# Kernel tuning notes

Hardware: AMD Instinct MI355X
Metric: run time of the kernel (lower is better)

Reference implementation:

```python
import jax, jax.numpy as jnp
import numpy as np

NC = 80
REG_MAX = 16
STRIDES = (8.0, 16.0, 32.0)
MAX_DET = 300
IOU_THR = 0.7
CONF_THR = 0.001
NCAND = 1024        # top candidates kept before greedy NMS
MAX_WH = 7680.0     # per-class offset trick (ultralytics max_wh)


def _make_anchors(shapes, strides, offset=0.5):
    pts, strs = [], []
    for (h, w), s in zip(shapes, strides):
        sx = jnp.arange(w, dtype=jnp.float32) + offset
        sy = jnp.arange(h, dtype=jnp.float32) + offset
        gy, gx = jnp.meshgrid(sy, sx, indexing='ij')
        pts.append(jnp.stack((gx, gy), -1).reshape(-1, 2))   # (h*w, 2)
        strs.append(jnp.full((h * w, 1), s, jnp.float32))
    return jnp.concatenate(pts, 0), jnp.concatenate(strs, 0)


def _decode_raw(feats):
    """feats_to_raw_yolov8: DFL decode + anchor transform -> pixel cxcywh + sigmoid cls."""
    B = feats[0].shape[0]
    no = 4 * REG_MAX + NC
    merged = jnp.concatenate([f.reshape(B, no, -1) for f in feats], axis=2)  # (B,no,A)
    dist, cls = merged[:, :4 * REG_MAX], merged[:, 4 * REG_MAX:]
    pd = dist.transpose(0, 2, 1).reshape(B, -1, 4, REG_MAX)                  # (B,A,4,reg_max)
    proj = jnp.arange(REG_MAX, dtype=merged.dtype)
    ltrb = jnp.einsum('bafr,r->baf', jax.nn.softmax(pd, -1), proj)           # (B,A,4)
    anchors, strd = _make_anchors([f.shape[2:] for f in feats], STRIDES)     # (A,2),(A,1)
    lt, rb = ltrb[..., :2], ltrb[..., 2:]
    x1y1 = anchors[None] - lt
    x2y2 = anchors[None] + rb
    cxy = (x1y1 + x2y2) * 0.5
    wh = x2y2 - x1y1
    dbox = jnp.concatenate((cxy, wh), -1) * strd[None]                       # (B,A,4) pixel cxcywh
    return dbox, jax.nn.sigmoid(cls).transpose(0, 2, 1)                      # (B,A,nc)


def _iou_one_vs_many(box, boxes):
    lt = jnp.maximum(box[:2], boxes[:, :2])
    rb = jnp.minimum(box[2:], boxes[:, 2:])
    inter = jnp.prod(jnp.clip(rb - lt, 0.0), -1)
    a1 = jnp.prod(box[2:] - box[:2])
    a2 = jnp.prod(boxes[:, 2:] - boxes[:, :2], -1)
    return inter / (a1 + a2 - inter + 1e-7)


def _nms_image(boxes_cxcywh, scores_cls):
    """conf threshold + per-class greedy NMS + max_det truncation -> (max_det, 6)."""
    conf = scores_cls.max(-1)                                   # (A,)
    cls = jnp.argmax(scores_cls, -1).astype(jnp.float32)        # (A,)
    conf = jnp.where(conf > CONF_THR, conf, 0.0)
    top_conf, idx = jax.lax.top_k(conf, NCAND)                  # candidate pre-selection
    cb = boxes_cxcywh[idx]                                      # (NCAND,4) cxcywh
    ccls = cls[idx]
    xy1 = cb[:, :2] - cb[:, 2:] * 0.5
    xy2 = cb[:, :2] + cb[:, 2:] * 0.5
    bx = jnp.concatenate((xy1, xy2), -1) + (ccls * MAX_WH)[:, None]  # class-offset xyxy

    def step(sc, _):
        j = jnp.argmax(sc)
        s = sc[j]
        sup = _iou_one_vs_many(bx[j], bx) > IOU_THR  # self-IoU=1 kills j as well
        return jnp.where(sup, 0.0, sc), (j, s)

    _, (sel, ss) = jax.lax.scan(step, top_conf, None, length=MAX_DET)
    rows = jnp.concatenate((cb[sel], ss[:, None], ccls[sel][:, None]), -1)  # (max_det,6)
    return jnp.where((ss > CONF_THR)[:, None], rows, 0.0)


def setup_inputs() -> dict:
    key = jax.random.key(0)
    k0, k1, k2 = jax.random.split(key, 3)
    B, no = 32, 4 * REG_MAX + NC
    return {
        'feat0': jax.random.normal(k0, (B, no, 80, 80), jnp.float32),
        'feat1': jax.random.normal(k1, (B, no, 40, 40), jnp.float32),
        'feat2': jax.random.normal(k2, (B, no, 20, 20), jnp.float32),
    }


def reference(feat0, feat1, feat2):
    dbox, ps = _decode_raw([feat0, feat1, feat2])        # (B,A,4), (B,A,nc)
    return jax.vmap(_nms_image)(dbox, ps)                # (B, max_det, 6)
```

## Files before the change

kernel.cpp:

```cpp
#include <hip/hip_runtime.h>
#include <stdint.h>

#define NCLS    80
#define NA_TOT  8400
#define NBATCH  32
#define MAXDET  300
#define SSORT   2048
#define RANKCAP 1536
#define CONFTHR 0.001f
#define TILES_PER_IMG 132

__device__ __forceinline__ float xla_expf(float in) {
  const float exp_hi = 88.3762626647950f;
  const float exp_lo = -88.3762626647949f;
  const float LOG2EF = 1.44269504088896341f;
  const float C1 = 0.693359375f;
  const float C2 = -2.12194440e-4f;
  const float p0 = 1.9875691500E-4f, p1 = 1.3981999507E-3f, p2 = 8.3334519073E-3f;
  const float p3 = 4.1665795894E-2f, p4 = 1.6666665459E-1f, p5 = 5.0000001201E-1f;
  float x = fminf(fmaxf(in, exp_lo), exp_hi);
  float fx = floorf(__fadd_rn(__fmul_rn(x, LOG2EF), 0.5f));
  float tmp = __fmul_rn(C1, fx);
  float z   = __fmul_rn(C2, fx);
  x = __fsub_rn(x, tmp);
  x = __fsub_rn(x, z);
  float y = __fadd_rn(__fmul_rn(x, p0), p1);
  y = __fadd_rn(__fmul_rn(y, x), p2);
  y = __fadd_rn(__fmul_rn(y, x), p3);
  y = __fadd_rn(__fmul_rn(y, x), p4);
  y = __fadd_rn(__fmul_rn(y, x), p5);
  y = __fadd_rn(__fmul_rn(y, __fmul_rn(x, x)), x);
  y = __fadd_rn(1.0f, y);
  int m = (int)fx;
  float s = __uint_as_float((uint32_t)(m + 127) << 23);
  float r = __fmul_rn(y, s);
  return fmaxf(r, in);
}

__device__ __forceinline__ float xla_sigmoid(float v) {
  float e = xla_expf(-v);
  float den = __fadd_rn(1.0f, e);
  return 1.0f / den;
}

__device__ __forceinline__ void gload_lds16(const float* gp, float* lp) {
  __builtin_amdgcn_global_load_lds(
      (const __attribute__((address_space(1))) void*)gp,
      (__attribute__((address_space(3))) void*)lp, 16, 0, 0);
}

__global__ __launch_bounds__(256) void yolo_decode_kernel(
    const float* __restrict__ f0, const float* __restrict__ f1,
    const float* __restrict__ f2,
    float4* __restrict__ oboxes, float* __restrict__ oconf,
    float* __restrict__ oclsf) {
  __shared__ float sm[144 * 64];
  int bx  = blockIdx.x;
  int b   = bx / TILES_PER_IMG;
  int r   = bx - b * TILES_PER_IMG;
  int tid = threadIdx.x;
  int lane = tid & 63;
  int wv   = tid >> 6;

  const float* base; int Alvl, W, a0, lvlbase; float stridef;
  if (r < 100)      { base = f0 + (size_t)b * (144 * 6400); W = 80; Alvl = 6400;
                      a0 = r * 64; stridef = 8.0f; lvlbase = 0; }
  else if (r < 125) { base = f1 + (size_t)b * (144 * 1600); W = 40; Alvl = 1600;
                      a0 = (r - 100) * 64; stridef = 16.0f; lvlbase = 6400; }
  else              { base = f2 + (size_t)b * (144 * 400);  W = 20; Alvl = 400;
                      int aa = (r - 125) * 64; a0 = (aa + 64 <= 400) ? aa : 336;
                      stridef = 32.0f; lvlbase = 8000; }

  #pragma unroll
  for (int qq = 0; qq < 9; ++qq) {
    int chunk = wv * 9 + qq;
    int c     = chunk * 4 + (lane >> 4);
    int s     = (c >> 4) & 3;
    int idx4  = (lane & 15) ^ (s << 2);
    const float* gp = base + (size_t)c * Alvl + a0 + idx4 * 4;
    gload_lds16(gp, sm + chunk * 256);
  }
  asm volatile("s_waitcnt vmcnt(0)" ::: "memory");
  __builtin_amdgcn_s_barrier();

  const float* S = sm;
  int idx = tid >> 2;
  int w   = tid & 3;
  int ai  = a0 + idx;
  float ax = __fadd_rn((float)(ai % W), 0.5f);
  float ay = __fadd_rn((float)(ai / W), 0.5f);

  int sidx = idx ^ (w << 4);
  float d[16];
  float mx = -INFINITY;
  #pragma unroll
  for (int rr = 0; rr < 16; ++rr) {
    d[rr] = S[(w * 16 + rr) * 64 + sidx];
    mx = fmaxf(mx, d[rr]);
  }
  float e[16]; float ssum = 0.0f;
  #pragma unroll
  for (int rr = 0; rr < 16; ++rr) {
    e[rr] = xla_expf(__fsub_rn(d[rr], mx));
    ssum = __fadd_rn(ssum, e[rr]);
  }
  float acc = 0.0f;
  #pragma unroll
  for (int rr = 0; rr < 16; ++rr) {
    float p = e[rr] / ssum;
    acc = __fadd_rn(acc, __fmul_rn(p, (float)rr));
  }

  int l0 = lane & ~3;
  float lt0 = __shfl(acc, l0 + 0);
  float lt1 = __shfl(acc, l0 + 1);
  float lt2 = __shfl(acc, l0 + 2);
  float lt3 = __shfl(acc, l0 + 3);

  float best = -INFINITY, second = -INFINITY; int bi = 0;
  #pragma unroll 5
  for (int kk = 0; kk < 20; ++kk) {
    int c = 64 + w * 20 + kk;
    float v = S[c * 64 + (idx ^ (((c >> 4) & 3) << 4))];
    if (v > best)        { second = best; best = v; bi = w * 20 + kk; }
    else if (v > second) { second = v; }
  }
  float gb = __shfl(best, l0 + 0), gs = __shfl(second, l0 + 0);
  int   gi = __shfl(bi,   l0 + 0);
  #pragma unroll
  for (int qq = 1; qq < 4; ++qq) {
    float bq = __shfl(best, l0 + qq), sq = __shfl(second, l0 + qq);
    int   iq = __shfl(bi,   l0 + qq);
    if (bq > gb) { gs = fmaxf(gb, sq); gb = bq; gi = iq; }
    else         { gs = fmaxf(gs, bq); }
  }

  float conf = 0.0f; int cls = gi;
  if (__fsub_rn(gb, gs) < 1e-4f || gb > 5.0f) {
    if (w == 0) {
      float bs = -INFINITY; int bj = 0;
      for (int kk = 0; kk < NCLS; ++kk) {
        int c = 64 + kk;
        float v = S[c * 64 + (idx ^ (((c >> 4) & 3) << 4))];
        float s2 = xla_sigmoid(v);
        if (s2 > bs) { bs = s2; bj = kk; }
      }
      conf = bs; cls = bj;
    }
  } else {
    conf = xla_sigmoid(gb);
  }

  if (w == 0) {
    float x1 = __fsub_rn(ax, lt0);
    float y1 = __fsub_rn(ay, lt1);
    float x2 = __fadd_rn(ax, lt2);
    float y2 = __fadd_rn(ay, lt3);
    float cx = __fmul_rn(__fadd_rn(x1, x2), 0.5f);
    float cy = __fmul_rn(__fadd_rn(y1, y2), 0.5f);
    float ww = __fsub_rn(x2, x1);
    float hh = __fsub_rn(y2, y1);
    int t = b * NA_TOT + lvlbase + a0 + idx;
    oboxes[t] = make_float4(__fmul_rn(cx, stridef), __fmul_rn(cy, stridef),
                            __fmul_rn(ww, stridef), __fmul_rn(hh, stridef));
    conf = (conf > CONFTHR) ? conf : 0.0f;
    oconf[t] = conf;
    oclsf[t] = (float)cls;
  }
}

struct __align__(16) K2Lds {
  unsigned long long sortkeys[SSORT];
  unsigned confL[NA_TOT];
  unsigned hist[16][257];
  unsigned tot[257];
  unsigned Tarr[257];
};

__global__ __launch_bounds__(1024) void yolo_select_kernel(
    const float4* __restrict__ boxes, const float* __restrict__ conf,
    const float* __restrict__ clsf,
    float* __restrict__ g_rowd, unsigned long long* __restrict__ g_clsMask) {
  __shared__ K2Lds u;
  __shared__ unsigned s_need, s_prefix, s_found, s_B, s_scnt, s_cut, s_done;
  int b    = blockIdx.x;
  int tid  = threadIdx.x;
  int lane = tid & 63;
  int wv   = tid >> 6;
  const unsigned* confu = (const unsigned*)conf + (size_t)b * NA_TOT;
  float* rowd = g_rowd + (size_t)b * 1024 * 8;
  unsigned long long* cm = g_clsMask + (size_t)b * (NCLS * 16);

  for (int i = tid; i < NA_TOT; i += 1024) u.confL[i] = confu[i];
  {
    float4 z4 = make_float4(0.f, 0.f, 0.f, 0.f);
    float4* gr = (float4*)rowd;
    for (int k = tid; k < 2048; k += 1024) gr[k] = z4;
  }
  for (int i = tid; i < NCLS * 16; i += 1024) cm[i] = 0ull;
  if (tid == 0) { s_need = 1024; s_prefix = 0; s_cut = 0; s_done = 0; s_scnt = 0; }
  __syncthreads();

  for (int lv = 0; lv < 4; ++lv) {
    __syncthreads();
    if (s_done) break;
    for (int i = tid; i < 16 * 257; i += 1024) ((unsigned*)u.hist)[i] = 0;
    if (tid == 0) { s_found = 0; s_B = 0; }
    __syncthreads();
    unsigned pfx = s_prefix;
    for (int it = 0; it < 9; ++it) {
      int i = tid + it * 1024;
      unsigned c = (i < NA_TOT) ? u.confL[i] : 0u;
      bool in; unsigned bin;
      if (lv == 0)      { in = true;                bin = c >> 23; }
      else if (lv == 1) { in = ((c >> 23) == pfx);  bin = (c >> 15) & 0xFF; }
      else if (lv == 2) { in = ((c >> 15) == pfx);  bin = (c >> 7) & 0xFF; }
      else              { in = ((c >> 7)  == pfx);  bin = c & 0x7F; }
      bool act = (c != 0) && in;
      unsigned long long ab = __ballot(act);
      if (ab) {
        int fl = __ffsll(ab) - 1;
        unsigned fbin = __shfl(bin, fl);
        unsigned long long same = __ballot(act && (bin == fbin));
        if (same == ab) {
          if (lane == fl) atomicAdd(&u.hist[wv][fbin], (unsigned)__popcll(ab));
        } else if (act) {
          atomicAdd(&u.hist[wv][bin], 1u);
        }
      }
    }
    __syncthreads();
    if (tid < 256) {
      unsigned s = 0;
      #pragma unroll
      for (int q = 0; q < 16; ++q) s += u.hist[q][tid];
      u.tot[tid] = s;
    }
    __syncthreads();
    if (tid < 64) {
      unsigned carry = 0;
      if (tid == 0) u.Tarr[256] = 0;
      for (int ch = 3; ch >= 0; --ch) {
        int bb = ch * 64 + tid;
        unsigned v = u.tot[bb];
        #pragma unroll
        for (int off = 1; off < 64; off <<= 1) {
          unsigned t2 = __shfl_down(v, off);
          if (tid + off < 64) v += t2;
        }
        u.Tarr[bb] = v + carry;
        carry += __shfl(v, 0);
      }
    }
    __syncthreads();
    unsigned need = s_need;
    if (tid < 256) {
      unsigned h = u.tot[tid];
      if (h > 0 && u.Tarr[tid + 1] < need && u.Tarr[tid + 1] + h >= need) {
        s_B = (unsigned)tid; s_found = 1;
      }
    }
    __syncthreads();
    if (tid == 0) {
      if (!s_found) { s_cut = 1; s_done = 1; }
      else {
        unsigned B = s_B;
        unsigned selcnt = (1024u - need) + u.Tarr[B];
        if (selcnt <= (unsigned)RANKCAP || lv == 3) {
          s_done = 1;
          if (lv == 0)      s_cut = B << 23;
          else if (lv == 1) s_cut = (s_prefix << 23) | (B << 15);
          else if (lv == 2) s_cut = (s_prefix << 15) | (B << 7);
          else              s_cut = (s_prefix << 7)  | B;
        } else {
          s_need   = need - u.Tarr[B + 1];
          s_prefix = (s_prefix << 8) | B;
        }
      }
    }
  }
  __syncthreads();

  unsigned cut = s_cut;
  for (int it = 0; it < 9; ++it) {
    int i = tid + it * 1024;
    unsigned c = (i < NA_TOT) ? u.confL[i] : 0u;
    bool sel = (c != 0 && c >= cut);
    unsigned long long bal = __ballot(sel);
    unsigned base2 = 0;
    if (lane == 0 && bal) base2 = atomicAdd(&s_scnt, (unsigned)__popcll(bal));
    base2 = __shfl(base2, 0);
    if (sel) {
      unsigned p = base2 + (unsigned)__popcll(bal & ((1ull << lane) - 1ull));
      if (p < SSORT)
        u.sortkeys[p] = ((unsigned long long)c << 32) |
                        (unsigned long long)(0xFFFFFFFFu - (unsigned)i);
    }
  }
  __syncthreads();
  unsigned scnt = s_scnt; if (scnt > SSORT) scnt = SSORT;
  unsigned snp = (scnt + 1u) & ~1u;
  if (tid == 0 && (scnt & 1u)) u.sortkeys[scnt] = 0ull;
  __syncthreads();

  for (unsigned e = tid; e < scnt; e += 1024) {
    unsigned long long mykey = u.sortkeys[e];
    unsigned r = 0;
    #pragma unroll 4
    for (unsigned j = 0; j < snp; j += 2) {
      ulonglong2 kk = *reinterpret_cast<const ulonglong2*>(&u.sortkeys[j]);
      r += (kk.x > mykey) ? 1u : 0u;
      r += (kk.y > mykey) ? 1u : 0u;
    }
    if (r < 1024) {
      unsigned a = 0xFFFFFFFFu - (unsigned)(mykey & 0xFFFFFFFFull);
      float4 cb = boxes[(size_t)b * NA_TOT + a];
      float cls = clsf[(size_t)b * NA_TOT + a];
      float4* gr = (float4*)(rowd + (size_t)r * 8);
      gr[0] = cb;
      gr[1] = make_float4(__uint_as_float((unsigned)(mykey >> 32)), cls, 0.f, 0.f);
      atomicOr(&cm[(int)cls * 16 + (r >> 6)], 1ull << (r & 63));
    }
  }
}

struct K3Lds {
  unsigned long long rows[1024][16];
  float    rowdata[1024][6];
  unsigned long long am[16];
};

__global__ __launch_bounds__(1024) void yolo_nms_kernel(
    const float* __restrict__ g_rowd,
    const unsigned long long* __restrict__ g_clsMask,
    float* __restrict__ out) {
  __shared__ K3Lds u;
  __shared__ unsigned s_sticky, s_fill;
  int b    = blockIdx.x;
  int tid  = threadIdx.x;
  const unsigned long long* cm = g_clsMask + (size_t)b * (NCLS * 16);

  {
    const float4* gr = (const float4*)(g_rowd + ((size_t)b * 1024 + tid) * 8);
    float4 v0 = gr[0];
    float4 v1 = gr[1];
    u.rowdata[tid][0] = v0.x; u.rowdata[tid][1] = v0.y;
    u.rowdata[tid][2] = v0.z; u.rowdata[tid][3] = v0.w;
    u.rowdata[tid][4] = v1.x; u.rowdata[tid][5] = v1.y;
  }
  {
    unsigned long long* flat = &u.rows[0][0];
    for (int k = tid; k < 1024 * 16; k += 1024) flat[k] = 0ull;
  }
  if (tid < 16) u.am[tid] = 0ull;
  if (tid == 0) { s_sticky = 0xFFFFFFFFu; s_fill = 0; }
  __syncthreads();

  {
    float cls = u.rowdata[tid][5];
    int c = (int)cls;
    const unsigned long long* cmask = cm + c * 16;
    bool valid = (cmask[tid >> 6] >> (tid & 63)) & 1ull;
    if (valid) {
      float bx0 = u.rowdata[tid][0], by0 = u.rowdata[tid][1];
      float bw0 = u.rowdata[tid][2], bh0 = u.rowdata[tid][3];
      float off = __fmul_rn(cls, 7680.0f);
      float hw  = __fmul_rn(bw0, 0.5f), hh = __fmul_rn(bh0, 0.5f);
      float wx1 = __fadd_rn(__fsub_rn(bx0, hw), off);
      float wy1 = __fadd_rn(__fsub_rn(by0, hh), off);
      float wx2 = __fadd_rn(__fadd_rn(bx0, hw), off);
      float wy2 = __fadd_rn(__fadd_rn(by0, hh), off);
      float a1  = __fmul_rn(__fsub_rn(wx2, wx1), __fsub_rn(wy2, wy1));
      int sw = tid & 15;
      for (int q = 0; q < 16; ++q) {
        unsigned long long m = cmask[q];
        while (m) {
          int bit = __ffsll(m) - 1;
          m &= m - 1ull;
          int j = q * 64 + bit;
          float jx = u.rowdata[j][0], jy = u.rowdata[j][1];
          float jw = u.rowdata[j][2], jh = u.rowdata[j][3];
          float jhw = __fmul_rn(jw, 0.5f), jhh = __fmul_rn(jh, 0.5f);
          float jx1 = __fadd_rn(__fsub_rn(jx, jhw), off);
          float jy1 = __fadd_rn(__fsub_rn(jy, jhh), off);
          float jx2 = __fadd_rn(__fadd_rn(jx, jhw), off);
          float jy2 = __fadd_rn(__fadd_rn(jy, jhh), off);
          float ltx = fmaxf(wx1, jx1), lty = fmaxf(wy1, jy1);
          float rbx = fminf(wx2, jx2), rby = fminf(wy2, jy2);
          float iw = fmaxf(__fsub_rn(rbx, ltx), 0.0f);
          float ih = fmaxf(__fsub_rn(rby, lty), 0.0f);
          float inter = __fmul_rn(iw, ih);
          float a2 = __fmul_rn(__fsub_rn(jx2, jx1), __fsub_rn(jy2, jy1));
          float den = __fadd_rn(__fsub_rn(__fadd_rn(a1, a2), inter), 1e-7f);
          float iou = inter / den;
          if (iou > 0.7f)
            u.rows[tid][(j >> 6) ^ sw] |= (1ull << (j & 63));
        }
      }
    }
  }
  __syncthreads();

  if (tid < NCLS) {
    const unsigned long long* cmask = cm + tid * 16;
    unsigned long long alive[16];
    bool any = false;
    #pragma unroll
    for (int q = 0; q < 16; ++q) { alive[q] = cmask[q]; any |= (alive[q] != 0ull); }
    while (any) {
      int r = -1;
      #pragma unroll
      for (int q = 0; q < 16; ++q)
        if (r < 0 && alive[q]) r = q * 64 + (__ffsll(alive[q]) - 1);
      atomicOr(&u.am[r >> 6], 1ull << (r & 63));
      int sw = r & 15;
      unsigned long long selfw = u.rows[r][(r >> 6) ^ sw];
      bool selfbit = (selfw >> (r & 63)) & 1ull;
      if (!selfbit) { atomicMin(&s_sticky, (unsigned)r); break; }
      any = false;
      #pragma unroll
      for (int q = 0; q < 16; ++q) {
        alive[q] &= ~u.rows[r][q ^ sw];
        any |= (alive[q] != 0ull);
      }
    }
  }
  __syncthreads();

  unsigned rs = s_sticky;
  {
    unsigned r = (unsigned)tid;
    bool surv = (u.am[r >> 6] >> (r & 63)) & 1ull;
    if (surv && r <= rs) {
      unsigned e2 = 0;
      int hi = (int)(r >> 6);
      #pragma unroll
      for (int q = 0; q < 16; ++q) {
        unsigned long long m = u.am[q];
        if (q < hi)       e2 += (unsigned)__popcll(m);
        else if (q == hi) e2 += (unsigned)__popcll(m & ((1ull << (r & 63)) - 1ull));
      }
      if (e2 < MAXDET) {
        float* orow = out + (size_t)b * (MAXDET * 6) + (size_t)e2 * 6;
        orow[0] = u.rowdata[r][0];
        orow[1] = u.rowdata[r][1];
        orow[2] = u.rowdata[r][2];
        orow[3] = u.rowdata[r][3];
        orow[4] = u.rowdata[r][4];
        orow[5] = u.rowdata[r][5];
      }
    }
  }
  if (tid == 0) {
    unsigned fill;
    if (rs != 0xFFFFFFFFu) {
      unsigned es = 0;
      int hi = (int)(rs >> 6);
      #pragma unroll
      for (int q = 0; q < 16; ++q) {
        unsigned long long m = u.am[q];
        if (q < hi)       es += (unsigned)__popcll(m);
        else if (q == hi) es += (unsigned)__popcll(m & ((1ull << (rs & 63)) - 1ull));
      }
      fill = es + 1;
    } else {
      unsigned S = 0;
      #pragma unroll
      for (int q = 0; q < 16; ++q) S += (unsigned)__popcll(u.am[q]);
      fill = S;
    }
    s_fill = (fill > (unsigned)MAXDET) ? (unsigned)MAXDET : fill;
  }
  __syncthreads();

  {
    unsigned fill = s_fill;
    bool st = (rs != 0xFFFFFFFFu);
    float* orow = out + (size_t)b * (MAXDET * 6);
    for (int i = (int)fill * 6 + tid; i < MAXDET * 6; i += 1024) {
      float v = 0.0f;
      if (st) v = u.rowdata[rs][i - (i / 6) * 6];
      orow[i] = v;
    }
  }
}

extern "C" void kernel_launch(void* const* d_in, const int* in_sizes, int n_in,
                              void* d_out, int out_size, void* d_ws, size_t ws_size,
                              hipStream_t stream) {
  const float* f0 = (const float*)d_in[0];
  const float* f1 = (const float*)d_in[1];
  const float* f2 = (const float*)d_in[2];
  float* out = (float*)d_out;

  char* ws = (char*)d_ws;
  float4* boxes = (float4*)ws;
  float*  conf  = (float*)(ws + (size_t)NBATCH * NA_TOT * 16);
  float*  clsf  = (float*)(ws + (size_t)NBATCH * NA_TOT * 20);
  float*  rowd  = (float*)(ws + (size_t)NBATCH * NA_TOT * 24);
  unsigned long long* clsm =
      (unsigned long long*)(ws + (size_t)NBATCH * NA_TOT * 24 + 1048576);

  yolo_decode_kernel<<<NBATCH * TILES_PER_IMG, 256, 0, stream>>>(
      f0, f1, f2, boxes, conf, clsf);
  yolo_select_kernel<<<NBATCH, 1024, 0, stream>>>(boxes, conf, clsf, rowd, clsm);
  yolo_nms_kernel<<<NBATCH, 1024, 0, stream>>>(rowd, clsm, out);
}
```

Baseline: 136.8 us.

## Split rank-sort of candidates into separate kernel across 8 blocks per image

The O(n^2) rank counting of selected candidate keys moves out of the single-block-per-image select kernel into a new kernel that launches 8 blocks of 256 threads per image. Keys pass through a global workspace buffer instead of LDS. This spreads the quadratic ranking over many more CUs than the original 32 blocks could use. The cost is an extra kernel launch and key comparisons read from global memory or cache instead of LDS.

```diff
diff --git a/kernel.cpp b/kernel.cpp
--- a/kernel.cpp
+++ b/kernel.cpp
@@ -9,6 +9,7 @@
 #define RANKCAP 1536
 #define CONFTHR 0.001f
 #define TILES_PER_IMG 132
+#define GKCAP   2056
 
 __device__ __forceinline__ float xla_expf(float in) {
   const float exp_hi = 88.3762626647950f;
@@ -170,7 +171,6 @@
 }
 
 struct __align__(16) K2Lds {
-  unsigned long long sortkeys[SSORT];
   unsigned confL[NA_TOT];
   unsigned hist[16][257];
   unsigned tot[257];
@@ -178,8 +178,8 @@
 };
 
 __global__ __launch_bounds__(1024) void yolo_select_kernel(
-    const float4* __restrict__ boxes, const float* __restrict__ conf,
-    const float* __restrict__ clsf,
+    const float* __restrict__ conf,
+    unsigned long long* __restrict__ g_keys, unsigned* __restrict__ g_scnt,
     float* __restrict__ g_rowd, unsigned long long* __restrict__ g_clsMask) {
   __shared__ K2Lds u;
   __shared__ unsigned s_need, s_prefix, s_found, s_B, s_scnt, s_cut, s_done;
@@ -188,16 +188,16 @@
   int lane = tid & 63;
   int wv   = tid >> 6;
   const unsigned* confu = (const unsigned*)conf + (size_t)b * NA_TOT;
-  float* rowd = g_rowd + (size_t)b * 1024 * 8;
-  unsigned long long* cm = g_clsMask + (size_t)b * (NCLS * 16);
+  unsigned long long* gk = g_keys + (size_t)b * GKCAP;
 
   for (int i = tid; i < NA_TOT; i += 1024) u.confL[i] = confu[i];
   {
     float4 z4 = make_float4(0.f, 0.f, 0.f, 0.f);
-    float4* gr = (float4*)rowd;
+    float4* gr = (float4*)(g_rowd + (size_t)b * 1024 * 8);
     for (int k = tid; k < 2048; k += 1024) gr[k] = z4;
   }
-  for (int i = tid; i < NCLS * 16; i += 1024) cm[i] = 0ull;
+  for (int i = tid; i < NCLS * 16; i += 1024)
+    g_clsMask[(size_t)b * (NCLS * 16) + i] = 0ull;
   if (tid == 0) { s_need = 1024; s_prefix = 0; s_cut = 0; s_done = 0; s_scnt = 0; }
   __syncthreads();
 
@@ -293,34 +293,51 @@
     if (sel) {
       unsigned p = base2 + (unsigned)__popcll(bal & ((1ull << lane) - 1ull));
       if (p < SSORT)
-        u.sortkeys[p] = ((unsigned long long)c << 32) |
-                        (unsigned long long)(0xFFFFFFFFu - (unsigned)i);
-    }
-  }
-  __syncthreads();
-  unsigned scnt = s_scnt; if (scnt > SSORT) scnt = SSORT;
-  unsigned snp = (scnt + 1u) & ~1u;
-  if (tid == 0 && (scnt & 1u)) u.sortkeys[scnt] = 0ull;
-  __syncthreads();
-
-  for (unsigned e = tid; e < scnt; e += 1024) {
-    unsigned long long mykey = u.sortkeys[e];
-    unsigned r = 0;
-    #pragma unroll 4
-    for (unsigned j = 0; j < snp; j += 2) {
-      ulonglong2 kk = *reinterpret_cast<const ulonglong2*>(&u.sortkeys[j]);
-      r += (kk.x > mykey) ? 1u : 0u;
-      r += (kk.y > mykey) ? 1u : 0u;
-    }
-    if (r < 1024) {
-      unsigned a = 0xFFFFFFFFu - (unsigned)(mykey & 0xFFFFFFFFull);
-      float4 cb = boxes[(size_t)b * NA_TOT + a];
-      float cls = clsf[(size_t)b * NA_TOT + a];
-      float4* gr = (float4*)(rowd + (size_t)r * 8);
-      gr[0] = cb;
-      gr[1] = make_float4(__uint_as_float((unsigned)(mykey >> 32)), cls, 0.f, 0.f);
-      atomicOr(&cm[(int)cls * 16 + (r >> 6)], 1ull << (r & 63));
-    }
+        gk[p] = ((unsigned long long)c << 32) |
+                (unsigned long long)(0xFFFFFFFFu - (unsigned)i);
+    }
+  }
+  __syncthreads();
+  if (tid == 0) {
+    unsigned sc = s_scnt; if (sc > SSORT) sc = SSORT;
+    g_scnt[b] = sc;
+    if (sc & 1u) gk[sc] = 0ull;
+  }
+}
+
+__global__ __launch_bounds__(256) void yolo_rank_kernel(
+    const unsigned long long* __restrict__ g_keys,
+    const unsigned* __restrict__ g_scnt,
+    const float4* __restrict__ boxes, const float* __restrict__ clsf,
+    float* __restrict__ g_rowd, unsigned long long* __restrict__ g_clsMask) {
+  int bx   = blockIdx.x;
+  int b    = bx >> 3;
+  int part = bx & 7;
+  const unsigned long long* gk = g_keys + (size_t)b * GKCAP;
+  unsigned scnt = g_scnt[b];
+  unsigned snp  = (scnt + 1u) & ~1u;
+  unsigned e    = (unsigned)(part * 256 + threadIdx.x);
+  bool has = (e < scnt);
+  unsigned long long mykey = has ? gk[e] : 0ull;
+
+  unsigned r = 0;
+  #pragma unroll 4
+  for (unsigned j = 0; j < snp; j += 2) {
+    ulonglong2 kk = *reinterpret_cast<const ulonglong2*>(gk + j);
+    r += (kk.x > mykey) ? 1u : 0u;
+    r += (kk.y > mykey) ? 1u : 0u;
+  }
+
+  if (has && r < 1024) {
+    unsigned a = 0xFFFFFFFFu - (unsigned)(mykey & 0xFFFFFFFFull);
+    float4 cb = boxes[(size_t)b * NA_TOT + a];
+    float cls = clsf[(size_t)b * NA_TOT + a];
+    float* rowd = g_rowd + (size_t)b * 1024 * 8;
+    float4* gr = (float4*)(rowd + (size_t)r * 8);
+    gr[0] = cb;
+    gr[1] = make_float4(__uint_as_float((unsigned)(mykey >> 32)), cls, 0.f, 0.f);
+    atomicOr(&g_clsMask[(size_t)b * (NCLS * 16) + (int)cls * 16 + (r >> 6)],
+             1ull << (r & 63));
   }
 }
 
@@ -497,12 +514,17 @@
   float4* boxes = (float4*)ws;
   float*  conf  = (float*)(ws + (size_t)NBATCH * NA_TOT * 16);
   float*  clsf  = (float*)(ws + (size_t)NBATCH * NA_TOT * 20);
-  float*  rowd  = (float*)(ws + (size_t)NBATCH * NA_TOT * 24);
-  unsigned long long* clsm =
-      (unsigned long long*)(ws + (size_t)NBATCH * NA_TOT * 24 + 1048576);
+  size_t off = (size_t)NBATCH * NA_TOT * 24;
+  float*  rowd  = (float*)(ws + off);                 off += 1048576;
+  unsigned long long* clsm = (unsigned long long*)(ws + off); off += 327680;
+  unsigned long long* gkeys = (unsigned long long*)(ws + off); off += (size_t)NBATCH * GKCAP * 8;
+  unsigned* scnts = (unsigned*)(ws + off);
 
   yolo_decode_kernel<<<NBATCH * TILES_PER_IMG, 256, 0, stream>>>(
       f0, f1, f2, boxes, conf, clsf);
-  yolo_select_kernel<<<NBATCH, 1024, 0, stream>>>(boxes, conf, clsf, rowd, clsm);
+  yolo_select_kernel<<<NBATCH, 1024, 0, stream>>>(conf, gkeys, scnts,
+                                                  rowd, clsm);
+  yolo_rank_kernel<<<NBATCH * 8, 256, 0, stream>>>(gkeys, scnts, boxes, clsf,
+                                                   rowd, clsm);
   yolo_nms_kernel<<<NBATCH, 1024, 0, stream>>>(rowd, clsm, out);
 }
```

Result: slower. 152.0 us (+11.1%).

## Defer DFL box decode to only the top-1024 selected candidates

Applied to the files above, without the earlier changes.

The first kernel now reads only the 80 class channels and writes conf/class, skipping the 64 DFL distance channels for all 8400 anchors. A new kernel after selection runs the softmax-DFL decode only for the kept candidates, reading their 64 channels with strided gathers, and writes the box into the row buffer. The select kernel stores the anchor index in place of the box. This cuts decode-stage HBM traffic and exp work by roughly 44%, at the cost of an extra launch and uncoalesced per-candidate gathers.

```diff
diff --git a/kernel.cpp b/kernel.cpp
--- a/kernel.cpp
+++ b/kernel.cpp
@@ -49,12 +49,11 @@
       (__attribute__((address_space(3))) void*)lp, 16, 0, 0);
 }
 
-__global__ __launch_bounds__(256) void yolo_decode_kernel(
+__global__ __launch_bounds__(256) void yolo_confcls_kernel(
     const float* __restrict__ f0, const float* __restrict__ f1,
     const float* __restrict__ f2,
-    float4* __restrict__ oboxes, float* __restrict__ oconf,
-    float* __restrict__ oclsf) {
-  __shared__ float sm[144 * 64];
+    float* __restrict__ oconf, float* __restrict__ oclsf) {
+  __shared__ float sm[80 * 64];
   int bx  = blockIdx.x;
   int b   = bx / TILES_PER_IMG;
   int r   = bx - b * TILES_PER_IMG;
@@ -62,23 +61,22 @@
   int lane = tid & 63;
   int wv   = tid >> 6;
 
-  const float* base; int Alvl, W, a0, lvlbase; float stridef;
-  if (r < 100)      { base = f0 + (size_t)b * (144 * 6400); W = 80; Alvl = 6400;
-                      a0 = r * 64; stridef = 8.0f; lvlbase = 0; }
-  else if (r < 125) { base = f1 + (size_t)b * (144 * 1600); W = 40; Alvl = 1600;
-                      a0 = (r - 100) * 64; stridef = 16.0f; lvlbase = 6400; }
-  else              { base = f2 + (size_t)b * (144 * 400);  W = 20; Alvl = 400;
+  const float* base; int Alvl, a0, lvlbase;
+  if (r < 100)      { base = f0 + (size_t)b * (144 * 6400); Alvl = 6400;
+                      a0 = r * 64; lvlbase = 0; }
+  else if (r < 125) { base = f1 + (size_t)b * (144 * 1600); Alvl = 1600;
+                      a0 = (r - 100) * 64; lvlbase = 6400; }
+  else              { base = f2 + (size_t)b * (144 * 400);  Alvl = 400;
                       int aa = (r - 125) * 64; a0 = (aa + 64 <= 400) ? aa : 336;
-                      stridef = 32.0f; lvlbase = 8000; }
+                      lvlbase = 8000; }
 
   #pragma unroll
-  for (int qq = 0; qq < 9; ++qq) {
-    int chunk = wv * 9 + qq;
+  for (int qq = 0; qq < 5; ++qq) {
+    int chunk = wv * 5 + qq;
     int c     = chunk * 4 + (lane >> 4);
     int s     = (c >> 4) & 3;
     int idx4  = (lane & 15) ^ (s << 2);
-    const float* gp = base + (size_t)c * Alvl + a0 + idx4 * 4;
-    gload_lds16(gp, sm + chunk * 256);
+    gload_lds16(base + (size_t)(64 + c) * Alvl + a0 + idx4 * 4, sm + chunk * 256);
   }
   asm volatile("s_waitcnt vmcnt(0)" ::: "memory");
   __builtin_amdgcn_s_barrier();
@@ -86,45 +84,16 @@
   const float* S = sm;
   int idx = tid >> 2;
   int w   = tid & 3;
-  int ai  = a0 + idx;
-  float ax = __fadd_rn((float)(ai % W), 0.5f);
-  float ay = __fadd_rn((float)(ai / W), 0.5f);
-
-  int sidx = idx ^ (w << 4);
-  float d[16];
-  float mx = -INFINITY;
-  #pragma unroll
-  for (int rr = 0; rr < 16; ++rr) {
-    d[rr] = S[(w * 16 + rr) * 64 + sidx];
-    mx = fmaxf(mx, d[rr]);
-  }
-  float e[16]; float ssum = 0.0f;
-  #pragma unroll
-  for (int rr = 0; rr < 16; ++rr) {
-    e[rr] = xla_expf(__fsub_rn(d[rr], mx));
-    ssum = __fadd_rn(ssum, e[rr]);
-  }
-  float acc = 0.0f;
-  #pragma unroll
-  for (int rr = 0; rr < 16; ++rr) {
-    float p = e[rr] / ssum;
-    acc = __fadd_rn(acc, __fmul_rn(p, (float)rr));
-  }
-
-  int l0 = lane & ~3;
-  float lt0 = __shfl(acc, l0 + 0);
-  float lt1 = __shfl(acc, l0 + 1);
-  float lt2 = __shfl(acc, l0 + 2);
-  float lt3 = __shfl(acc, l0 + 3);
 
   float best = -INFINITY, second = -INFINITY; int bi = 0;
   #pragma unroll 5
   for (int kk = 0; kk < 20; ++kk) {
-    int c = 64 + w * 20 + kk;
+    int c = w * 20 + kk;
     float v = S[c * 64 + (idx ^ (((c >> 4) & 3) << 4))];
-    if (v > best)        { second = best; best = v; bi = w * 20 + kk; }
+    if (v > best)        { second = best; best = v; bi = c; }
     else if (v > second) { second = v; }
   }
+  int l0 = lane & ~3;
   float gb = __shfl(best, l0 + 0), gs = __shfl(second, l0 + 0);
   int   gi = __shfl(bi,   l0 + 0);
   #pragma unroll
@@ -140,8 +109,7 @@
     if (w == 0) {
       float bs = -INFINITY; int bj = 0;
       for (int kk = 0; kk < NCLS; ++kk) {
-        int c = 64 + kk;
-        float v = S[c * 64 + (idx ^ (((c >> 4) & 3) << 4))];
+        float v = S[kk * 64 + (idx ^ (((kk >> 4) & 3) << 4))];
         float s2 = xla_sigmoid(v);
         if (s2 > bs) { bs = s2; bj = kk; }
       }
@@ -152,17 +120,7 @@
   }
 
   if (w == 0) {
-    float x1 = __fsub_rn(ax, lt0);
-    float y1 = __fsub_rn(ay, lt1);
-    float x2 = __fadd_rn(ax, lt2);
-    float y2 = __fadd_rn(ay, lt3);
-    float cx = __fmul_rn(__fadd_rn(x1, x2), 0.5f);
-    float cy = __fmul_rn(__fadd_rn(y1, y2), 0.5f);
-    float ww = __fsub_rn(x2, x1);
-    float hh = __fsub_rn(y2, y1);
     int t = b * NA_TOT + lvlbase + a0 + idx;
-    oboxes[t] = make_float4(__fmul_rn(cx, stridef), __fmul_rn(cy, stridef),
-                            __fmul_rn(ww, stridef), __fmul_rn(hh, stridef));
     conf = (conf > CONFTHR) ? conf : 0.0f;
     oconf[t] = conf;
     oclsf[t] = (float)cls;
@@ -178,8 +136,7 @@
 };
 
 __global__ __launch_bounds__(1024) void yolo_select_kernel(
-    const float4* __restrict__ boxes, const float* __restrict__ conf,
-    const float* __restrict__ clsf,
+    const float* __restrict__ conf, const float* __restrict__ clsf,
     float* __restrict__ g_rowd, unsigned long long* __restrict__ g_clsMask) {
   __shared__ K2Lds u;
   __shared__ unsigned s_need, s_prefix, s_found, s_B, s_scnt, s_cut, s_done;
@@ -314,14 +271,72 @@
     }
     if (r < 1024) {
       unsigned a = 0xFFFFFFFFu - (unsigned)(mykey & 0xFFFFFFFFull);
-      float4 cb = boxes[(size_t)b * NA_TOT + a];
       float cls = clsf[(size_t)b * NA_TOT + a];
       float4* gr = (float4*)(rowd + (size_t)r * 8);
-      gr[0] = cb;
-      gr[1] = make_float4(__uint_as_float((unsigned)(mykey >> 32)), cls, 0.f, 0.f);
+      gr[1] = make_float4(__uint_as_float((unsigned)(mykey >> 32)), cls,
+                          __uint_as_float(a), 0.f);
       atomicOr(&cm[(int)cls * 16 + (r >> 6)], 1ull << (r & 63));
     }
   }
+}
+
+__global__ __launch_bounds__(128) void yolo_dfl_kernel(
+    const float* __restrict__ f0, const float* __restrict__ f1,
+    const float* __restrict__ f2, float* __restrict__ g_rowd) {
+  int bx   = blockIdx.x;
+  int b    = bx >> 3;
+  int part = bx & 7;
+  int r    = part * 128 + threadIdx.x;
+  float* rd = g_rowd + ((size_t)b * 1024 + r) * 8;
+  float conf = rd[4];
+  if (conf == 0.0f) return;
+  unsigned a = __float_as_uint(rd[6]);
+
+  const float* base; int ai, W; float stridef;
+  if (a < 6400)      { base = f0 + (size_t)b * (144 * 6400); ai = a;        W = 80; stridef = 8.0f;  }
+  else if (a < 8000) { base = f1 + (size_t)b * (144 * 1600); ai = a - 6400; W = 40; stridef = 16.0f; }
+  else               { base = f2 + (size_t)b * (144 * 400);  ai = a - 8000; W = 20; stridef = 32.0f; }
+  int Alvl = W * W;
+  const float* cptr = base + ai;
+  float ax = __fadd_rn((float)(ai % W), 0.5f);
+  float ay = __fadd_rn((float)(ai / W), 0.5f);
+
+  float ltrb[4];
+  #pragma unroll
+  for (int fs = 0; fs < 4; ++fs) {
+    float d[16];
+    float mx = -INFINITY;
+    #pragma unroll
+    for (int rr = 0; rr < 16; ++rr) {
+      d[rr] = cptr[(size_t)(fs * 16 + rr) * Alvl];
+      mx = fmaxf(mx, d[rr]);
+    }
+    float e[16]; float ssum = 0.0f;
+    #pragma unroll
+    for (int rr = 0; rr < 16; ++rr) {
+      e[rr] = xla_expf(__fsub_rn(d[rr], mx));
+      ssum = __fadd_rn(ssum, e[rr]);
+    }
+    float acc = 0.0f;
+    #pragma unroll
+    for (int rr = 0; rr < 16; ++rr) {
+      float p = e[rr] / ssum;
+      acc = __fadd_rn(acc, __fmul_rn(p, (float)rr));
+    }
+    ltrb[fs] = acc;
+  }
+
+  float x1 = __fsub_rn(ax, ltrb[0]);
+  float y1 = __fsub_rn(ay, ltrb[1]);
+  float x2 = __fadd_rn(ax, ltrb[2]);
+  float y2 = __fadd_rn(ay, ltrb[3]);
+  float cx = __fmul_rn(__fadd_rn(x1, x2), 0.5f);
+  float cy = __fmul_rn(__fadd_rn(y1, y2), 0.5f);
+  float w  = __fsub_rn(x2, x1);
+  float h  = __fsub_rn(y2, y1);
+  *reinterpret_cast<float4*>(rd) =
+      make_float4(__fmul_rn(cx, stridef), __fmul_rn(cy, stridef),
+                  __fmul_rn(w, stridef),  __fmul_rn(h, stridef));
 }
 
 struct K3Lds {
@@ -494,15 +509,15 @@
   float* out = (float*)d_out;
 
   char* ws = (char*)d_ws;
-  float4* boxes = (float4*)ws;
-  float*  conf  = (float*)(ws + (size_t)NBATCH * NA_TOT * 16);
-  float*  clsf  = (float*)(ws + (size_t)NBATCH * NA_TOT * 20);
-  float*  rowd  = (float*)(ws + (size_t)NBATCH * NA_TOT * 24);
-  unsigned long long* clsm =
-      (unsigned long long*)(ws + (size_t)NBATCH * NA_TOT * 24 + 1048576);
-
-  yolo_decode_kernel<<<NBATCH * TILES_PER_IMG, 256, 0, stream>>>(
-      f0, f1, f2, boxes, conf, clsf);
-  yolo_select_kernel<<<NBATCH, 1024, 0, stream>>>(boxes, conf, clsf, rowd, clsm);
+  float* conf = (float*)ws;
+  float* clsf = (float*)(ws + (size_t)NBATCH * NA_TOT * 4);
+  size_t off  = (size_t)NBATCH * NA_TOT * 8;
+  float* rowd = (float*)(ws + off);             off += 1048576;
+  unsigned long long* clsm = (unsigned long long*)(ws + off);
+
+  yolo_confcls_kernel<<<NBATCH * TILES_PER_IMG, 256, 0, stream>>>(
+      f0, f1, f2, conf, clsf);
+  yolo_select_kernel<<<NBATCH, 1024, 0, stream>>>(conf, clsf, rowd, clsm);
+  yolo_dfl_kernel<<<NBATCH * 8, 128, 0, stream>>>(f0, f1, f2, rowd);
   yolo_nms_kernel<<<NBATCH, 1024, 0, stream>>>(rowd, clsm, out);
 }
```

New measurement: 154.9 us. 1.13x slower.

## Give each wave a private 16-anchor LDS slice and drop the block barrier

Applied to the files above, without the earlier changes.

The decode kernel now has each wave load its own 16 anchors across all 144 channels into a private LDS region, instead of the whole block cooperatively loading 64 anchors into a shared swizzled tile. This removes the block-wide s_barrier, since a wave only waits on its own loads, and it drops the XOR swizzle indexing. Lanes are remapped so that the four DFL sides sit 16 lanes apart, which changes the shuffle patterns. Global reads become 64-byte contiguous segments per channel instead of 256-byte ones, which may reduce coalescing efficiency. LDS reads may also see more bank conflicts now that the swizzle is gone.

```diff
diff --git a/kernel.cpp b/kernel.cpp
--- a/kernel.cpp
+++ b/kernel.cpp
@@ -54,7 +54,7 @@
     const float* __restrict__ f2,
     float4* __restrict__ oboxes, float* __restrict__ oconf,
     float* __restrict__ oclsf) {
-  __shared__ float sm[144 * 64];
+  __shared__ float sm[4 * 144 * 16];
   int bx  = blockIdx.x;
   int b   = bx / TILES_PER_IMG;
   int r   = bx - b * TILES_PER_IMG;
@@ -71,31 +71,29 @@
                       int aa = (r - 125) * 64; a0 = (aa + 64 <= 400) ? aa : 336;
                       stridef = 32.0f; lvlbase = 8000; }
 
+  int a0w = a0 + wv * 16;
+  float* Sw = sm + wv * (144 * 16);
+
   #pragma unroll
-  for (int qq = 0; qq < 9; ++qq) {
-    int chunk = wv * 9 + qq;
-    int c     = chunk * 4 + (lane >> 4);
-    int s     = (c >> 4) & 3;
-    int idx4  = (lane & 15) ^ (s << 2);
-    const float* gp = base + (size_t)c * Alvl + a0 + idx4 * 4;
-    gload_lds16(gp, sm + chunk * 256);
+  for (int k = 0; k < 9; ++k) {
+    int ch = k * 16 + (lane >> 2);
+    const float* gp = base + (size_t)ch * Alvl + a0w + (lane & 3) * 4;
+    gload_lds16(gp, Sw + k * 256);
   }
   asm volatile("s_waitcnt vmcnt(0)" ::: "memory");
-  __builtin_amdgcn_s_barrier();
-
-  const float* S = sm;
-  int idx = tid >> 2;
-  int w   = tid & 3;
-  int ai  = a0 + idx;
+  __builtin_amdgcn_sched_barrier(0);
+
+  int idx = lane & 15;
+  int w   = lane >> 4;
+  int ai  = a0w + idx;
   float ax = __fadd_rn((float)(ai % W), 0.5f);
   float ay = __fadd_rn((float)(ai / W), 0.5f);
 
-  int sidx = idx ^ (w << 4);
   float d[16];
   float mx = -INFINITY;
   #pragma unroll
   for (int rr = 0; rr < 16; ++rr) {
-    d[rr] = S[(w * 16 + rr) * 64 + sidx];
+    d[rr] = Sw[(w * 16 + rr) * 16 + idx];
     mx = fmaxf(mx, d[rr]);
   }
   float e[16]; float ssum = 0.0f;
@@ -111,26 +109,25 @@
     acc = __fadd_rn(acc, __fmul_rn(p, (float)rr));
   }
 
-  int l0 = lane & ~3;
-  float lt0 = __shfl(acc, l0 + 0);
-  float lt1 = __shfl(acc, l0 + 1);
-  float lt2 = __shfl(acc, l0 + 2);
-  float lt3 = __shfl(acc, l0 + 3);
+  float lt0 = __shfl(acc, idx + 0);
+  float lt1 = __shfl(acc, idx + 16);
+  float lt2 = __shfl(acc, idx + 32);
+  float lt3 = __shfl(acc, idx + 48);
 
   float best = -INFINITY, second = -INFINITY; int bi = 0;
   #pragma unroll 5
   for (int kk = 0; kk < 20; ++kk) {
     int c = 64 + w * 20 + kk;
-    float v = S[c * 64 + (idx ^ (((c >> 4) & 3) << 4))];
+    float v = Sw[c * 16 + idx];
     if (v > best)        { second = best; best = v; bi = w * 20 + kk; }
     else if (v > second) { second = v; }
   }
-  float gb = __shfl(best, l0 + 0), gs = __shfl(second, l0 + 0);
-  int   gi = __shfl(bi,   l0 + 0);
+  float gb = __shfl(best, idx + 0), gs = __shfl(second, idx + 0);
+  int   gi = __shfl(bi,   idx + 0);
   #pragma unroll
   for (int qq = 1; qq < 4; ++qq) {
-    float bq = __shfl(best, l0 + qq), sq = __shfl(second, l0 + qq);
-    int   iq = __shfl(bi,   l0 + qq);
+    float bq = __shfl(best, idx + qq * 16), sq = __shfl(second, idx + qq * 16);
+    int   iq = __shfl(bi,   idx + qq * 16);
     if (bq > gb) { gs = fmaxf(gb, sq); gb = bq; gi = iq; }
     else         { gs = fmaxf(gs, bq); }
   }
@@ -140,8 +137,7 @@
     if (w == 0) {
       float bs = -INFINITY; int bj = 0;
       for (int kk = 0; kk < NCLS; ++kk) {
-        int c = 64 + kk;
-        float v = S[c * 64 + (idx ^ (((c >> 4) & 3) << 4))];
+        float v = Sw[(64 + kk) * 16 + idx];
         float s2 = xla_sigmoid(v);
         if (s2 > bs) { bs = s2; bj = kk; }
       }
@@ -160,7 +156,7 @@
     float cy = __fmul_rn(__fadd_rn(y1, y2), 0.5f);
     float ww = __fsub_rn(x2, x1);
     float hh = __fsub_rn(y2, y1);
-    int t = b * NA_TOT + lvlbase + a0 + idx;
+    int t = b * NA_TOT + lvlbase + a0w + idx;
     oboxes[t] = make_float4(__fmul_rn(cx, stridef), __fmul_rn(cy, stridef),
                             __fmul_rn(ww, stridef), __fmul_rn(hh, stridef));
     conf = (conf > CONFTHR) ? conf : 0.0f;
```

Result: no change. 135.7 us (-0.8%).
